# Optimization experiments

Measured on AMD Instinct MI355X. Metric: run time of the kernel, lower is better.

The kernel has to match this reference:

```python
import math
import jax, jax.numpy as jnp
import numpy as np

B, S, D, H = 2, 2048, 1024, 16
HD = D // H  # 64


def setup_inputs() -> dict:
    key = jax.random.key(0)
    k = jax.random.split(key, 8)
    x = jax.random.normal(k[0], (B, S, D), dtype=jnp.float32)
    # RoPE tables: inv_freq over half dim, emb = concat(freqs, freqs)
    inv_freq = 1.0 / (10000.0 ** (jnp.arange(0, HD, 2, dtype=jnp.float32) / HD))
    pos = jnp.arange(S, dtype=jnp.float32)
    freqs = pos[:, None] * inv_freq[None, :]            # [S, HD/2]
    emb = jnp.concatenate([freqs, freqs], axis=-1)      # [S, HD]
    cos = jnp.cos(emb)[:, None, :]                      # [S, 1, HD] broadcasts over [B,S,H,HD]
    sin = jnp.sin(emb)[:, None, :]
    # causal additive mask [1, 1, S, S]
    neg = jnp.finfo(jnp.float32).min
    mask = jnp.where(jnp.tril(jnp.ones((S, S), dtype=bool)), 0.0, neg)[None, None]
    scale = 0.02
    wq = jax.random.normal(k[1], (D, D), dtype=jnp.float32) * scale
    wk = jax.random.normal(k[2], (D, D), dtype=jnp.float32) * scale
    wv = jax.random.normal(k[3], (D, D), dtype=jnp.float32) * scale
    wo = jax.random.normal(k[4], (D, D), dtype=jnp.float32) * scale
    return {"x": x, "cos": cos, "sin": sin, "mask": mask,
            "wq": wq, "wk": wk, "wv": wv, "wo": wo}


def rotate_half(t):
    t1, t2 = t[..., : t.shape[-1] // 2], t[..., t.shape[-1] // 2:]
    return jnp.concatenate([-t2, t1], axis=-1)


def reference(x, cos, sin, mask, wq, wk, wv, wo):
    b, s, d = x.shape
    # torch nn.Linear: y = x @ W^T  (W is [out, in])
    q = (x @ wq.T).reshape(b, s, H, HD)
    kk = (x @ wk.T).reshape(b, s, H, HD)
    v = (x @ wv.T).reshape(b, s, H, HD)
    q = q * cos + rotate_half(q) * sin
    kk = kk * cos + rotate_half(kk) * sin
    q = q.transpose(0, 2, 1, 3)   # [b, h, s, hd]
    kk = kk.transpose(0, 2, 1, 3)
    v = v.transpose(0, 2, 1, 3)
    scores = jnp.einsum('bhqd,bhkd->bhqk', q, kk) / math.sqrt(HD)
    scores = scores + mask
    probs = jax.nn.softmax(scores.astype(jnp.float32), axis=-1).astype(q.dtype)
    out = jnp.einsum('bhqk,bhkd->bhqd', probs, v)
    out = out.transpose(0, 2, 1, 3).reshape(b, s, d)
    return out @ wo.T
```

## Files before the change

### kernel.cpp

```cpp
#include <hip/hip_runtime.h>
#include <hip/hip_bf16.h>

typedef __hip_bfloat16 bf16;
typedef unsigned short u16;
typedef __attribute__((ext_vector_type(8))) short short8;
typedef __attribute__((ext_vector_type(4))) float floatx4;

constexpr int B_ = 2, S_ = 2048, D_ = 1024, H_ = 16, HD_ = 64;
constexpr int KT = 64, PAD = 72;
constexpr int GK = 1024, BK = 64;

__device__ inline float b2f(u16 u) {
    union { unsigned int i; float f; } v; v.i = ((unsigned int)u) << 16; return v.f;
}
__device__ inline u16 f2b(float f) {
    bf16 h = __float2bfloat16(f); return *(u16*)&h;
}

__device__ inline void gl16(const u16* g, u16* l) {
    __builtin_amdgcn_global_load_lds(
        (const __attribute__((address_space(1))) unsigned int*)g,
        (__attribute__((address_space(3))) unsigned int*)l, 16, 0, 0);
}

#define SBAR() __builtin_amdgcn_sched_barrier(0)

__global__ __launch_bounds__(256) void cvt_kernel(
    const float* __restrict__ x,  const float* __restrict__ wq,
    const float* __restrict__ wk, const float* __restrict__ wv,
    const float* __restrict__ wo,
    u16* __restrict__ Xb, u16* __restrict__ Wb)
{
    const size_t c = (size_t)blockIdx.x * 256 + threadIdx.x;
    const float* src; u16* dst; size_t off;
    if (c < (size_t)(1 << 19)) { src = x; dst = Xb; off = c; }
    else {
        const size_t w = c - (1 << 19);
        const int wi = (int)(w >> 17);
        off = w & ((1 << 17) - 1);
        src = (wi == 0) ? wq : (wi == 1) ? wk : (wi == 2) ? wv : wo;
        dst = Wb + ((size_t)wi << 20);
    }
    const float4 a = *(const float4*)(src + off * 8);
    const float4 b = *(const float4*)(src + off * 8 + 4);
    ushort4 u0; u0.x = f2b(a.x); u0.y = f2b(a.y); u0.z = f2b(a.z); u0.w = f2b(a.w);
    ushort4 u1; u1.x = f2b(b.x); u1.y = f2b(b.y); u1.z = f2b(b.z); u1.w = f2b(b.w);
    *(ushort4*)(dst + off * 8)     = u0;
    *(ushort4*)(dst + off * 8 + 4) = u1;
}

__global__ __launch_bounds__(512, 2) void qkv8(
    const u16* __restrict__ Ag, const u16* __restrict__ Wall,
    const float* __restrict__ cosp, const float* __restrict__ sinp,
    bf16* __restrict__ Qo, bf16* __restrict__ Ko, u16* __restrict__ Vt)
{
    extern __shared__ u16 lds[];

    const int wgid = (blockIdx.x & 7) * 24 + (blockIdx.x >> 3);
    const int mt = wgid / 12;
    const int rem = wgid - mt * 12;
    const int nt = rem & 3, z = rem >> 2;

    const u16* W = Wall + ((size_t)z << 20);
    const int m0 = mt * 256, n0 = nt * 256;

    const int tid  = threadIdx.x;
    const int wave = tid >> 6, lane = tid & 63;
    const int quad = lane >> 4, l16 = lane & 15;
    const int wm = wave >> 2, wn = wave & 3;

    const int lr_st = wave * 16 + (lane >> 2);
    const int csrc  = ((lane & 3) ^ ((lane >> 5) << 1)) * 8;
    const int grA   = ((lr_st >> 6) << 7) + (lr_st & 63);
    const int grB   = ((lr_st >> 5) << 6) + (lr_st & 31);

    const int cidx = ((quad ^ (((l16 >> 3) & 1) << 1))) * 8;

    floatx4 acc[8][4] = {};
    short8 af[4][2], bA[2][2], bB[2][2];

    const u16* A_st = Ag + (size_t)(m0 + grA) * GK + csrc;
    const u16* B_st = W  + (size_t)(n0 + grB) * GK + csrc;

    auto stA = [&](int t2, int mh) {
        const u16* s = A_st + ((size_t)mh * 64) * GK + t2 * 64;
        u16* d = lds + (((t2 & 1) * 2 + mh) * 8192) + wave * 512;
        gl16(s, d);
        gl16(s + 32, d + 4096);
    };
    auto stB = [&](int t2, int nh) {
        const u16* s = B_st + ((size_t)nh * 32) * GK + t2 * 64;
        u16* d = lds + 32768 + (((t2 & 1) * 2 + nh) * 8192) + wave * 512;
        gl16(s, d);
        gl16(s + 32, d + 4096);
    };
    auto rdA = [&](int sl, int mh) {
        const int base = (sl * 2 + mh) * 8192 + cidx;
#pragma unroll
        for (int mf = 0; mf < 4; ++mf) {
            const int lr = wm * 64 + mf * 16 + l16;
#pragma unroll
            for (int ks = 0; ks < 2; ++ks)
                af[mf][ks] = *(const short8*)&lds[base + ks * 4096 + lr * 32];
        }
    };
    auto rdB = [&](short8 (&bf)[2][2], int sl, int nh) {
        const int base = 32768 + (sl * 2 + nh) * 8192 + cidx;
#pragma unroll
        for (int fn = 0; fn < 2; ++fn) {
            const int lr = wn * 32 + fn * 16 + l16;
#pragma unroll
            for (int ks = 0; ks < 2; ++ks)
                bf[fn][ks] = *(const short8*)&lds[base + ks * 4096 + lr * 32];
        }
    };
    auto mm = [&](int mh, int nh, short8 (&bf)[2][2]) {
#pragma unroll
        for (int mf = 0; mf < 4; ++mf)
#pragma unroll
            for (int fn = 0; fn < 2; ++fn)
#pragma unroll
                for (int ks = 0; ks < 2; ++ks)
                    acc[mh * 4 + mf][nh * 2 + fn] =
                        __builtin_amdgcn_mfma_f32_16x16x32_bf16(
                            af[mf][ks], bf[fn][ks],
                            acc[mh * 4 + mf][nh * 2 + fn], 0, 0, 0);
    };

    stA(0, 0); stA(0, 1); stB(0, 0); stB(0, 1);
    asm volatile("s_waitcnt vmcnt(0)" ::: "memory");
    SBAR(); __builtin_amdgcn_s_barrier(); SBAR();

    for (int t = 0; t < 16; ++t) {
        const int sl = t & 1;
        if (t < 15) {
            stA(t + 1, 0); stA(t + 1, 1); stB(t + 1, 0); stB(t + 1, 1);
        }
        rdA(sl, 0); rdB(bA, sl, 0);
        mm(0, 0, bA);
        rdB(bB, sl, 1);
        mm(0, 1, bB);
        rdA(sl, 1);
        mm(1, 0, bA);
        mm(1, 1, bB);
        SBAR();
        if (t < 15) asm volatile("s_waitcnt vmcnt(0)" ::: "memory");
        __builtin_amdgcn_s_barrier();
        SBAR();
    }

    const int s0 = m0 & (S_ - 1);
    const int bq = m0 >> 11;
    const int h  = (n0 >> 6) + wn;

    if (z < 2) {
        float* Cs = (float*)lds;
        float* Sn = (float*)(lds + 16384);
        {
            const int rr = tid >> 1;
            const int cc = (tid & 1) * 16;
            const float4* cp = (const float4*)(cosp + (size_t)(s0 + rr) * HD_ + cc);
            const float4* sp = (const float4*)(sinp + (size_t)(s0 + rr) * HD_ + cc);
            float4* cd = (float4*)&Cs[rr * 32 + cc];
            float4* sd = (float4*)&Sn[rr * 32 + cc];
            cd[0] = cp[0]; cd[1] = cp[1]; cd[2] = cp[2]; cd[3] = cp[3];
            sd[0] = sp[0]; sd[1] = sp[1]; sd[2] = sp[2]; sd[3] = sp[3];
        }
        __syncthreads();

        const float scale = (z == 0) ? 0.125f * 1.44269504f : 1.0f;
        bf16* C = (z == 0) ? Qo : Ko;
#pragma unroll
        for (int mf = 0; mf < 8; ++mf)
#pragma unroll
            for (int r = 0; r < 4; ++r) {
                const int mr = wm * 128 + mf * 16 + quad * 4 + r;
                const size_t base = ((size_t)(bq * H_ + h) * S_ + s0 + mr) << 6;
#pragma unroll
                for (int np = 0; np < 2; ++np) {
                    const int d = np * 16 + l16;
                    const float c1 = Cs[mr * 32 + d];
                    const float s1 = Sn[mr * 32 + d];
                    const float q0 = acc[mf][np][r], q1 = acc[mf][np + 2][r];
                    C[base + d]      = __float2bfloat16((q0 * c1 - q1 * s1) * scale);
                    C[base + d + 32] = __float2bfloat16((q1 * c1 + q0 * s1) * scale);
                }
            }
    } else {
        const int bh = bq * H_ + h;
#pragma unroll
        for (int mf = 0; mf < 8; ++mf)
#pragma unroll
            for (int nf = 0; nf < 4; ++nf) {
                const int hd = nf * 16 + l16;
                const int sb = s0 + wm * 128 + mf * 16 + quad * 4;
                ushort4 pk;
                pk.x = f2b(acc[mf][nf][0]); pk.y = f2b(acc[mf][nf][1]);
                pk.z = f2b(acc[mf][nf][2]); pk.w = f2b(acc[mf][nf][3]);
                *(ushort4*)&Vt[((size_t)(bh * HD_ + hd) << 11) + sb] = pk;
            }
    }
}

template <typename TC, int SCATTER, int ROPE, int BN>
__global__ __launch_bounds__(256) void gemm_async(
    const u16* __restrict__ A, const u16* __restrict__ Wb,
    const float* __restrict__ cosp, const float* __restrict__ sinp,
    TC* __restrict__ C0, TC* __restrict__ C1, TC* __restrict__ C2, int N)
{
    constexpr int NT = BN / 32;

    int x, y, z;
    {
        const int xcd = blockIdx.x & 7, idx = blockIdx.x >> 3;
        y = (xcd & 3) * 8 + (idx & 7);
        if (BN == 128) {
            const int xz = (xcd >> 2) * 12 + (idx >> 3);
            x = xz & 7; z = xz >> 3;
        } else {
            x = (xcd >> 2) * 8 + (idx >> 3);
            z = 0;
        }
    }

    const u16* W = Wb + ((size_t)z << 20);
    TC*        C = (z == 0) ? C0 : (z == 1 ? C1 : C2);

    __shared__ __align__(16) u16 As[128 * BK];
    __shared__ __align__(16) u16 Bs[BN * BK];

    const int tid  = threadIdx.x;
    const int wave = tid >> 6, lane = tid & 63;
    const int quad = lane >> 4, l16 = lane & 15;
    const int wm = wave >> 1, wn = wave & 1;
    const int m0 = y * 128, n0 = x * BN;

    const int srl = lane >> 3;
    const int sc  = (lane & 7) ^ srl;

    floatx4 acc[4][NT] = {};

    for (int k0 = 0; k0 < GK; k0 += BK) {
        __syncthreads();
#pragma unroll
        for (int j = 0; j < 4; ++j) {
            const int rb = wave * 32 + j * 8;
            gl16(A + (size_t)(m0 + rb + srl) * GK + k0 + sc * 8, &As[rb * BK]);
        }
#pragma unroll
        for (int j = 0; j < BN / 32; ++j) {
            const int rb = wave * (BN / 4) + j * 8;
            gl16(W + (size_t)(n0 + rb + srl) * GK + k0 + sc * 8, &Bs[rb * BK]);
        }
        __syncthreads();

#pragma unroll
        for (int ks = 0; ks < 2; ++ks) {
            short8 af[4], bfr[NT];
#pragma unroll
            for (int mt = 0; mt < 4; ++mt) {
                const int R = wm * 64 + mt * 16 + l16;
                af[mt] = *(const short8*)&As[R * BK + (((ks * 4 + quad) ^ (l16 & 7)) * 8)];
            }
#pragma unroll
            for (int nt = 0; nt < NT; ++nt) {
                const int R = wn * (BN / 2) + nt * 16 + l16;
                bfr[nt] = *(const short8*)&Bs[R * BK + (((ks * 4 + quad) ^ (l16 & 7)) * 8)];
            }
#pragma unroll
            for (int mt = 0; mt < 4; ++mt)
#pragma unroll
                for (int nt = 0; nt < NT; ++nt)
                    acc[mt][nt] = __builtin_amdgcn_mfma_f32_16x16x32_bf16(
                        af[mt], bfr[nt], acc[mt][nt], 0, 0, 0);
        }
    }

    {
#pragma unroll
        for (int mt = 0; mt < 4; ++mt)
#pragma unroll
            for (int nt = 0; nt < NT; ++nt)
#pragma unroll
                for (int r = 0; r < 4; ++r) {
                    const int m = m0 + wm * 64 + mt * 16 + quad * 4 + r;
                    const int n = n0 + wn * (BN / 2) + nt * 16 + l16;
                    ((float*)C)[(size_t)m * N + n] = acc[mt][nt][r];
                }
    }
}

__global__ __launch_bounds__(256, 4) void fa_kernel(
    const u16* __restrict__ Qg, const u16* __restrict__ Kg, const u16* __restrict__ Vt,
    bf16* __restrict__ Og)
{
    __shared__ __align__(16) u16 Kt[2][KT * PAD];
    __shared__ __align__(16) u16 Vs[2][KT * PAD];

    const int flat = blockIdx.x;
    const int bh = flat & 31;
    const int rk = flat >> 5;
    const int g  = rk >> 3, j = rk & 7;
    const int qt = (g == 0) ? 31 - j : (g == 1) ? j : (g == 2) ? 23 - j : 8 + j;
    const int b  = bh >> 4, h = bh & 15;
    const int tid  = threadIdx.x;
    const int wave = tid >> 6, lane = tid & 63;
    const int quad = lane >> 4, l16 = lane & 15;
    const int srow = tid >> 2;
    const int sc4  = tid & 3;
    const int scol = sc4 * 16;
    const int vwb  = (sc4 >> 1) * 32 + (sc4 & 1) * 4;

    const int qrow0 = qt * 64 + wave * 16;

    union S8U { short8 v; ushort4 q[2]; };

    short8 aq0, aq1;
    {
        const u16* qrow = Qg + ((size_t)bh * S_ + qrow0 + l16) * HD_;
        aq0 = *(const short8*)(qrow + quad * 8);
        aq1 = *(const short8*)(qrow + 32 + quad * 8);
    }

    floatx4 oacc[4] = {};
    float lsum = 0.f;

    const int T = qt + 1;

    {
        const u16* kp = Kg + ((size_t)bh * S_ + srow) * HD_ + scol;
        *(short8*)&Kt[0][srow * PAD + scol]     = *(const short8*)kp;
        *(short8*)&Kt[0][srow * PAD + scol + 8] = *(const short8*)(kp + 8);
        const u16* vp = Vt + ((size_t)bh * HD_ + srow) * S_ + scol;
        S8U v0, v1; v0.v = *(const short8*)vp; v1.v = *(const short8*)(vp + 8);
        *(ushort4*)&Vs[0][srow * PAD + vwb]      = v0.q[0];
        *(ushort4*)&Vs[0][srow * PAD + vwb + 8]  = v0.q[1];
        *(ushort4*)&Vs[0][srow * PAD + vwb + 16] = v1.q[0];
        *(ushort4*)&Vs[0][srow * PAD + vwb + 24] = v1.q[1];
    }
    __syncthreads();

    for (int it = 0; it < T; ++it) {
        const int  cur = it & 1;
        const bool pf  = (it + 1 < T);
        short8 nk0, nk1; S8U nv0, nv1;
        if (pf) {
            const int kb2 = (it + 1) * KT;
            const u16* kp = Kg + ((size_t)bh * S_ + kb2 + srow) * HD_ + scol;
            nk0 = *(const short8*)kp; nk1 = *(const short8*)(kp + 8);
            const u16* vp = Vt + ((size_t)bh * HD_ + srow) * S_ + kb2 + scol;
            nv0.v = *(const short8*)vp; nv1.v = *(const short8*)(vp + 8);
        }

        floatx4 s0[4] = {{0,0,0,0},{0,0,0,0},{0,0,0,0},{0,0,0,0}};
        __builtin_amdgcn_s_setprio(1);
#pragma unroll
        for (int kt = 0; kt < 4; ++kt) {
            const short8 bk0 = *(const short8*)&Kt[cur][(kt * 16 + l16) * PAD + quad * 8];
            const short8 bk1 = *(const short8*)&Kt[cur][(kt * 16 + l16) * PAD + 32 + quad * 8];
            s0[kt] = __builtin_amdgcn_mfma_f32_16x16x32_bf16(bk0, aq0, s0[kt], 0, 0, 0);
            s0[kt] = __builtin_amdgcn_mfma_f32_16x16x32_bf16(bk1, aq1, s0[kt], 0, 0, 0);
        }
        __builtin_amdgcn_s_setprio(0);

        if (it == T - 1) {
            const int t0 = wave * 16 + l16 - quad * 4;
#pragma unroll
            for (int kt = 0; kt < 4; ++kt)
#pragma unroll
                for (int r = 0; r < 4; ++r)
                    if (kt * 16 + r > t0) s0[kt][r] = -1.0e38f;
        }

        short8 ah0, ah1;
        float rs = 0.f;
#pragma unroll
        for (int kt = 0; kt < 4; ++kt)
#pragma unroll
            for (int r = 0; r < 4; ++r) {
                const float e0 = __builtin_amdgcn_exp2f(s0[kt][r]);
                rs += e0;
                const int idx = (kt & 1) * 4 + r;
                if (kt < 2) ah0[idx] = (short)f2b(e0);
                else        ah1[idx] = (short)f2b(e0);
            }
        lsum += rs;

        __builtin_amdgcn_s_setprio(1);
#pragma unroll
        for (int dt = 0; dt < 4; ++dt) {
            const short8 bv0 = *(const short8*)&Vs[cur][(dt * 16 + l16) * PAD + quad * 8];
            const short8 bv1 = *(const short8*)&Vs[cur][(dt * 16 + l16) * PAD + 32 + quad * 8];
            oacc[dt] = __builtin_amdgcn_mfma_f32_16x16x32_bf16(bv0, ah0, oacc[dt], 0, 0, 0);
            oacc[dt] = __builtin_amdgcn_mfma_f32_16x16x32_bf16(bv1, ah1, oacc[dt], 0, 0, 0);
        }
        __builtin_amdgcn_s_setprio(0);

        if (pf) {
            const int nb = cur ^ 1;
            *(short8*)&Kt[nb][srow * PAD + scol]     = nk0;
            *(short8*)&Kt[nb][srow * PAD + scol + 8] = nk1;
            *(ushort4*)&Vs[nb][srow * PAD + vwb]      = nv0.q[0];
            *(ushort4*)&Vs[nb][srow * PAD + vwb + 8]  = nv0.q[1];
            *(ushort4*)&Vs[nb][srow * PAD + vwb + 16] = nv1.q[0];
            *(ushort4*)&Vs[nb][srow * PAD + vwb + 24] = nv1.q[1];
        }
        __syncthreads();
    }

    lsum += __shfl_xor(lsum, 16);
    lsum += __shfl_xor(lsum, 32);
    const float inv = 1.0f / lsum;
    bf16* orow = Og + ((size_t)(b * S_ + qrow0 + l16)) * D_ + h * HD_;
#pragma unroll
    for (int dt = 0; dt < 4; ++dt) {
        ushort4 pk;
        pk.x = f2b(oacc[dt][0] * inv);
        pk.y = f2b(oacc[dt][1] * inv);
        pk.z = f2b(oacc[dt][2] * inv);
        pk.w = f2b(oacc[dt][3] * inv);
        *(ushort4*)((u16*)orow + dt * 16 + quad * 4) = pk;
    }
}

extern "C" void kernel_launch(void* const* d_in, const int* in_sizes, int n_in,
                              void* d_out, int out_size, void* d_ws, size_t ws_size,
                              hipStream_t stream)
{
    const float* x    = (const float*)d_in[0];
    const float* cosp = (const float*)d_in[1];
    const float* sinp = (const float*)d_in[2];
    const float* wq   = (const float*)d_in[4];
    const float* wk   = (const float*)d_in[5];
    const float* wv   = (const float*)d_in[6];
    const float* wo   = (const float*)d_in[7];
    float* out = (float*)d_out;

    u16* w0 = (u16*)d_ws;
    const size_t NE = (size_t)B_ * S_ * D_;
    u16* Qb  = w0;
    u16* Kb  = w0 + NE;
    u16* Vtb = w0 + 2 * NE;
    u16* Xb  = w0 + 3 * NE;
    u16* Wb  = w0 + 4 * NE;
    u16* Ab  = Xb;
    u16* Wob = Wb + 3 * (1 << 20);

    static bool inited = false;
    if (!inited) {
        hipFuncSetAttribute((const void*)qkv8,
                            hipFuncAttributeMaxDynamicSharedMemorySize, 131072);
        inited = true;
    }

    cvt_kernel<<<4096, 256, 0, stream>>>(x, wq, wk, wv, wo, Xb, Wb);

    qkv8<<<192, 512, 131072, stream>>>(
        Xb, Wb, cosp, sinp, (bf16*)Qb, (bf16*)Kb, Vtb);

    fa_kernel<<<1024, 256, 0, stream>>>(Qb, Kb, Vtb, (bf16*)Ab);

    gemm_async<float, 0, 0, 64><<<512, 256, 0, stream>>>(
        Ab, Wob, cosp, sinp, out, out, out, D_);
}
```

Baseline: 174.8 us.

## Restructure QKV GEMM main loop into phased ping-pong schedule with setprio

Replaces the simple double-buffered K loop of the projection GEMM with a manually unrolled schedule. Each tile is split into four MFMA phases, and the global-to-LDS loads for the next tile are interleaved between them. Barriers, lgkmcnt waits and partial vmcnt(6) waits separate the phases, and s_setprio raises wave priority around the MFMA blocks. The aim is to hide global load latency and keep the matrix units busy, at the cost of many more barriers per tile and a fragile buffer-hazard schedule.

```diff
diff --git a/kernel.cpp b/kernel.cpp
--- a/kernel.cpp
+++ b/kernel.cpp
@@ -127,27 +127,65 @@
                             acc[mh * 4 + mf][nh * 2 + fn], 0, 0, 0);
     };
 
-    stA(0, 0); stA(0, 1); stB(0, 0); stB(0, 1);
-    asm volatile("s_waitcnt vmcnt(0)" ::: "memory");
+#define PH_SYNC()                                                       \
+    do { SBAR(); __builtin_amdgcn_s_barrier();                          \
+         asm volatile("s_waitcnt lgkmcnt(0)" ::: "memory"); SBAR(); } while (0)
+#define PH_END()                                                        \
+    do { SBAR(); __builtin_amdgcn_s_barrier(); SBAR(); } while (0)
+#define PH_END_V6()                                                     \
+    do { SBAR(); asm volatile("s_waitcnt vmcnt(6)" ::: "memory");       \
+         __builtin_amdgcn_s_barrier(); SBAR(); } while (0)
+#define PH_END_V0()                                                     \
+    do { SBAR(); asm volatile("s_waitcnt vmcnt(0)" ::: "memory");       \
+         __builtin_amdgcn_s_barrier(); SBAR(); } while (0)
+#define PRIO_MM(MH, NH, BF)                                             \
+    do { __builtin_amdgcn_s_setprio(1); mm(MH, NH, BF);                 \
+         __builtin_amdgcn_s_setprio(0); } while (0)
+
+    stA(0, 0); stB(0, 0); stA(0, 1); stB(0, 1); stA(1, 0); stB(1, 0); stA(1, 1);
+    asm volatile("s_waitcnt vmcnt(6)" ::: "memory");
     SBAR(); __builtin_amdgcn_s_barrier(); SBAR();
 
-    for (int t = 0; t < 16; ++t) {
-        const int sl = t & 1;
-        if (t < 15) {
-            stA(t + 1, 0); stA(t + 1, 1); stB(t + 1, 0); stB(t + 1, 1);
-        }
-        rdA(sl, 0); rdB(bA, sl, 0);
-        mm(0, 0, bA);
-        rdB(bB, sl, 1);
-        mm(0, 1, bB);
-        rdA(sl, 1);
-        mm(1, 0, bA);
-        mm(1, 1, bB);
-        SBAR();
-        if (t < 15) asm volatile("s_waitcnt vmcnt(0)" ::: "memory");
-        __builtin_amdgcn_s_barrier();
-        SBAR();
-    }
+    for (int i = 0; i < 7; ++i) {
+        const int t0 = 2 * i, t1 = 2 * i + 1;
+        rdA(0, 0); rdB(bA, 0, 0); stB(t1, 1);
+        PH_SYNC(); PRIO_MM(0, 0, bA); PH_END();
+        rdB(bB, 0, 1); stA(t0 + 2, 0);
+        PH_SYNC(); PRIO_MM(0, 1, bB); PH_END();
+        rdA(0, 1); stB(t0 + 2, 0);
+        PH_SYNC(); PRIO_MM(1, 0, bA); PH_END();
+        stA(t0 + 2, 1);
+        PH_SYNC(); PRIO_MM(1, 1, bB); PH_END_V6();
+        rdA(1, 0); rdB(bA, 1, 0); stB(t0 + 2, 1);
+        PH_SYNC(); PRIO_MM(0, 0, bA); PH_END();
+        rdB(bB, 1, 1); stA(t1 + 2, 0);
+        PH_SYNC(); PRIO_MM(0, 1, bB); PH_END();
+        rdA(1, 1); stB(t1 + 2, 0);
+        PH_SYNC(); PRIO_MM(1, 0, bA); PH_END();
+        stA(t1 + 2, 1);
+        PH_SYNC(); PRIO_MM(1, 1, bB); PH_END_V6();
+    }
+    {
+        rdA(0, 0); rdB(bA, 0, 0); stB(15, 1);
+        PH_SYNC(); PRIO_MM(0, 0, bA); PH_END();
+        rdB(bB, 0, 1);
+        PH_SYNC(); PRIO_MM(0, 1, bB); PH_END();
+        rdA(0, 1);
+        PH_SYNC(); PRIO_MM(1, 0, bA); PH_END();
+        PH_SYNC(); PRIO_MM(1, 1, bB); PH_END_V0();
+        rdA(1, 0); rdB(bA, 1, 0);
+        PH_SYNC(); PRIO_MM(0, 0, bA); PH_END();
+        rdB(bB, 1, 1);
+        PH_SYNC(); PRIO_MM(0, 1, bB); PH_END();
+        rdA(1, 1);
+        PH_SYNC(); PRIO_MM(1, 0, bA); PH_END();
+        PH_SYNC(); PRIO_MM(1, 1, bB); PH_END();
+    }
+#undef PH_SYNC
+#undef PH_END
+#undef PH_END_V6
+#undef PH_END_V0
+#undef PRIO_MM
 
     const int s0 = m0 & (S_ - 1);
     const int bq = m0 >> 11;
```

New measurement: 172.9 us. Within noise of the previous version (-1.1%).
